# Kernel optimization log

Hardware: AMD Instinct MI355X
Metric: run time of the kernel (lower is better)

The kernel has to match this reference:

```python
import jax, jax.numpy as jnp
import numpy as np

DIM, DK, DV = 1024, 128, 128

def setup_inputs() -> dict:
    key = jax.random.key(0)
    ks = jax.random.split(key, 7)
    X = jax.random.normal(ks[0], (4, 4096, DIM), dtype=jnp.float32)
    s = DIM ** -0.5
    Wq = jax.random.normal(ks[1], (DIM, DK), dtype=jnp.float32) * s
    bq = jnp.zeros((DK,), dtype=jnp.float32)
    Wk = jax.random.normal(ks[2], (DIM, DK), dtype=jnp.float32) * s
    bk = jnp.zeros((DK,), dtype=jnp.float32)
    Wv = jax.random.normal(ks[3], (DIM, DV), dtype=jnp.float32) * s
    bv = jnp.zeros((DV,), dtype=jnp.float32)
    return {"X": X, "Wq": Wq, "bq": bq, "Wk": Wk, "bk": bk, "Wv": Wv, "bv": bv}

def reference(X, Wq, bq, Wk, bk, Wv, bv):
    scale = DK ** -0.5
    q = X @ Wq + bq              # [B, S, dk]
    k = X @ Wk + bk              # [B, S, dk]
    v = X @ Wv + bv              # [B, S, dv]
    attn = jnp.einsum('bqd,bkd->bqk', q, k) * scale  # [B, S, S]
    attn = jax.nn.softmax(attn, axis=-1)
    return jnp.einsum('bqk,bkd->bqd', attn, v)       # [B, S, dv]
```

## Files before the change

kernel.cpp:

```cpp
#include <hip/hip_runtime.h>

#define NB 4
#define SEQ 4096
#define DIMK 1024
#define DKV 128
#define SCALE 0.08838834764831845f

typedef float  f32x4  __attribute__((ext_vector_type(4)));
typedef float  f32x16 __attribute__((ext_vector_type(16)));
typedef _Float16 f16x8 __attribute__((ext_vector_type(8)));

static __device__ __forceinline__ int pkrtz(float a, float b) {
    auto h = __builtin_amdgcn_cvt_pkrtz(a, b);
    return __builtin_bit_cast(int, h);
}

__global__ void prep_wt(const float* __restrict__ Wq, const float* __restrict__ Wk,
                        const float* __restrict__ Wv, _Float16* __restrict__ WT) {
    int tid = blockIdx.x * 256 + threadIdx.x;
    int n  = tid & 127;
    int k  = (tid >> 7) & 1023;
    int w3 = tid >> 17;
    const float* W = (w3 == 0) ? Wq : (w3 == 1) ? Wk : Wv;
    WT[((size_t)w3 * 128 + n) * 1024 + k] = (_Float16)W[(size_t)k * 128 + n];
}

__global__ __launch_bounds__(256) void qkv_proj(
    const float* __restrict__ X,
    const float* __restrict__ bq, const float* __restrict__ bk, const float* __restrict__ bv,
    const _Float16* __restrict__ WT,
    _Float16* __restrict__ Qh, _Float16* __restrict__ Kh, _Float16* __restrict__ VTh) {

    __shared__ __attribute__((aligned(16))) _Float16 WTs[128 * 40];
    const int t = threadIdx.x;
    const int w = t >> 6, l = t & 63;
    const int lrow = l & 15, lg = l >> 4;
    const int w3   = blockIdx.x % 3;
    const int tile = blockIdx.x / 3;
    const int r0 = tile * 64;

    f32x4 acc[8] = {};
    const float* xrow = X + (size_t)(r0 + w * 16 + lrow) * DIMK;
    const _Float16* Wbase = WT + (size_t)w3 * 128 * 1024;

    float4 xc0 = *(const float4*)(xrow + lg * 8);
    float4 xc1 = *(const float4*)(xrow + lg * 8 + 4);

    for (int k0 = 0; k0 < DIMK; k0 += 32) {
        __syncthreads();
        #pragma unroll
        for (int i = 0; i < 2; ++i) {
            int c = t + 256 * i;
            int row = c >> 2, part = c & 3;
            *(int4*)((char*)WTs + row * 80 + part * 16) =
                *(const int4*)(Wbase + (size_t)row * 1024 + k0 + part * 8);
        }
        float4 xn0, xn1;
        if (k0 + 32 < DIMK) {
            xn0 = *(const float4*)(xrow + k0 + 32 + lg * 8);
            xn1 = *(const float4*)(xrow + k0 + 32 + lg * 8 + 4);
        }
        __syncthreads();
        f16x8 a;
        a[0] = (_Float16)xc0.x; a[1] = (_Float16)xc0.y; a[2] = (_Float16)xc0.z; a[3] = (_Float16)xc0.w;
        a[4] = (_Float16)xc1.x; a[5] = (_Float16)xc1.y; a[6] = (_Float16)xc1.z; a[7] = (_Float16)xc1.w;

        #pragma unroll
        for (int n = 0; n < 8; ++n) {
            f16x8 bf = *(const f16x8*)((const char*)WTs + (n * 16 + lrow) * 80 + lg * 16);
            acc[n] = __builtin_amdgcn_mfma_f32_16x16x32_f16(a, bf, acc[n], 0, 0, 0);
        }
        xc0 = xn0; xc1 = xn1;
    }
    const float* bias = (w3 == 0) ? bq : (w3 == 1) ? bk : bv;
    #pragma unroll
    for (int n = 0; n < 8; ++n) {
        int col = n * 16 + lrow;
        float bv_ = bias[col];
        #pragma unroll
        for (int j = 0; j < 4; ++j) {
            int grow = r0 + w * 16 + lg * 4 + j;
            float val = acc[n][j] + bv_;
            if (w3 == 0) {
                Qh[(size_t)grow * DKV + col] = (_Float16)(val * SCALE);
            } else if (w3 == 1) {
                Kh[(size_t)grow * DKV + col] = (_Float16)val;
            } else {
                int b = grow >> 12, sp = grow & 4095;
                VTh[((size_t)b * DKV + col) * SEQ + sp] = (_Float16)val;
            }
        }
    }
}

__global__ __launch_bounds__(256, 2) void attn_kernel(
    const _Float16* __restrict__ Qh, const _Float16* __restrict__ Kh,
    const _Float16* __restrict__ VTh, float* __restrict__ out) {

    __shared__ __attribute__((aligned(16))) char lds[65536];

    const int t = threadIdx.x;
    const int w = t >> 6, l = t & 63;
    const int lq = l & 31;
    const int hi = l >> 5;
    const int g  = w >> 1;
    const int wg = w & 1;
    const int lt = t & 127;

    const int work = (blockIdx.x & 7) * 32 + (blockIdx.x >> 3);
    const int b  = work >> 6;
    const int qt = work & 63;
    const int q0 = qt * 64 + wg * 32;

    char* KsG = lds + g * 16384;
    char* VsG = lds + 32768 + g * 16384;

    f16x8 qf[8];
    #pragma unroll
    for (int c = 0; c < 8; ++c)
        qf[c] = *(const f16x8*)(Qh + (size_t)(b * SEQ + q0 + lq) * DKV + c * 16 + hi * 8);

    f32x16 o[4] = {};
    float m = -INFINITY, lsum = 0.f;

    for (int kt = 0; kt < 32; ++kt) {
        const int k0 = g * 2048 + kt * 64;
        __syncthreads();
        #pragma unroll
        for (int i = 0; i < 8; ++i) {
            int c = lt + 128 * i; int row = c >> 4, part = c & 15;
            *(int4*)(KsG + row * 256 + ((part * 16) ^ ((row & 7) << 4))) =
                *(const int4*)(Kh + (size_t)(b * SEQ + k0 + row) * DKV + part * 8);
        }
        #pragma unroll
        for (int i = 0; i < 8; ++i) {
            int c = lt + 128 * i; int dv = c >> 3, part = c & 7;
            *(int4*)(VsG + dv * 128 + ((part * 16) ^ ((dv & 7) << 4))) =
                *(const int4*)(VTh + (size_t)(b * DKV + dv) * SEQ + k0 + part * 8);
        }
        __syncthreads();

        f32x16 s0 = {}, s1 = {};
        #pragma unroll
        for (int c = 0; c < 8; ++c) {
            int col = c * 32 + hi * 16;
            f16x8 kf0 = *(const f16x8*)(KsG + lq * 256 + (col ^ ((lq & 7) << 4)));
            f16x8 kf1 = *(const f16x8*)(KsG + (32 + lq) * 256 + (col ^ ((lq & 7) << 4)));
            s0 = __builtin_amdgcn_mfma_f32_32x32x16_f16(kf0, qf[c], s0, 0, 0, 0);
            s1 = __builtin_amdgcn_mfma_f32_32x32x16_f16(kf1, qf[c], s1, 0, 0, 0);
        }

        float tm = -INFINITY;
        #pragma unroll
        for (int r = 0; r < 16; ++r) tm = fmaxf(tm, fmaxf(s0[r], s1[r]));
        tm = fmaxf(tm, __shfl_xor(tm, 32));

        if (__any(tm > m + 8.f)) {
            float mnew = fmaxf(m, tm);
            float corr = __expf(m - mnew);
            m = mnew;
            lsum *= corr;
            #pragma unroll
            for (int dvt = 0; dvt < 4; ++dvt) o[dvt] *= corr;
        }
        float ts = 0.f;
        #pragma unroll
        for (int r = 0; r < 16; ++r) { s0[r] = __expf(s0[r] - m); ts += s0[r]; }
        #pragma unroll
        for (int r = 0; r < 16; ++r) { s1[r] = __expf(s1[r] - m); ts += s1[r]; }
        ts += __shfl_xor(ts, 32);
        lsum += ts;

        int wv[16];
        #pragma unroll
        for (int i = 0; i < 8; ++i) wv[i]     = pkrtz(s0[2 * i], s0[2 * i + 1]);
        #pragma unroll
        for (int i = 0; i < 8; ++i) wv[8 + i] = pkrtz(s1[2 * i], s1[2 * i + 1]);

        #pragma unroll
        for (int s = 0; s < 4; ++s) {
            const int base = (s >> 1) * 8 + (s & 1) * 4;
            int x0 = __shfl_xor(wv[base + 0], 32);
            int x1 = __shfl_xor(wv[base + 1], 32);
            int x2 = __shfl_xor(wv[base + 2], 32);
            int x3 = __shfl_xor(wv[base + 3], 32);
            union { int i[4]; f16x8 v; } bu;
            bu.i[0] = hi ? x2 : wv[base + 0];
            bu.i[1] = hi ? x3 : wv[base + 1];
            bu.i[2] = hi ? wv[base + 2] : x0;
            bu.i[3] = hi ? wv[base + 3] : x1;
            #pragma unroll
            for (int dvt = 0; dvt < 4; ++dvt) {
                int row = dvt * 32 + lq;
                f16x8 vf = *(const f16x8*)(VsG + row * 128 +
                                           ((s * 32 + hi * 16) ^ ((row & 7) << 4)));
                o[dvt] = __builtin_amdgcn_mfma_f32_32x32x16_f16(vf, bu.v, o[dvt], 0, 0, 0);
            }
        }
    }

    float* obuf  = (float*)lds;
    float* mlbuf = (float*)(lds + 40960);

    __syncthreads();
    if (g == 1) {
        #pragma unroll
        for (int dvt = 0; dvt < 4; ++dvt)
            #pragma unroll
            for (int r = 0; r < 16; ++r)
                obuf[wg * 4096 + (dvt * 16 + r) * 64 + l] = o[dvt][r];
        if (l < 32) {
            mlbuf[(wg * 32 + l) * 2 + 0] = m;
            mlbuf[(wg * 32 + l) * 2 + 1] = lsum;
        }
    }
    __syncthreads();
    if (g == 0) {
        float mo  = mlbuf[(wg * 32 + lq) * 2 + 0];
        float lo_ = mlbuf[(wg * 32 + lq) * 2 + 1];
        float mn = fmaxf(m, mo);
        float ca = __expf(m - mn);
        float cb = __expf(mo - mn);
        float rl = 1.0f / (lsum * ca + lo_ * cb);
        #pragma unroll
        for (int dvt = 0; dvt < 4; ++dvt)
            #pragma unroll
            for (int r = 0; r < 16; ++r)
                o[dvt][r] = (o[dvt][r] * ca + obuf[wg * 4096 + (dvt * 16 + r) * 64 + l] * cb) * rl;
    }
    __syncthreads();
    float* tbuf = (float*)lds;
    if (g == 0) {
        #pragma unroll
        for (int dvt = 0; dvt < 4; ++dvt)
            #pragma unroll
            for (int r = 0; r < 16; ++r) {
                int dv = dvt * 32 + (r & 3) + 8 * (r >> 2) + 4 * hi;
                tbuf[(wg * 32 + lq) * 132 + dv] = o[dvt][r];
            }
    }
    __syncthreads();
    const size_t obase = (size_t)(b * SEQ + qt * 64) * DKV;
    int row = t >> 2, c0 = (t & 3) * 32;
    #pragma unroll
    for (int i = 0; i < 8; ++i) {
        float4 v = *(const float4*)(tbuf + row * 132 + c0 + i * 4);
        *(float4*)(out + obase + row * 128 + c0 + i * 4) = v;
    }
}

extern "C" void kernel_launch(void* const* d_in, const int* in_sizes, int n_in,
                              void* d_out, int out_size, void* d_ws, size_t ws_size,
                              hipStream_t stream) {
    const float* X  = (const float*)d_in[0];
    const float* Wq = (const float*)d_in[1];
    const float* bq = (const float*)d_in[2];
    const float* Wk = (const float*)d_in[3];
    const float* bk = (const float*)d_in[4];
    const float* Wv = (const float*)d_in[5];
    const float* bv = (const float*)d_in[6];
    float* out = (float*)d_out;

    const size_t nqe = (size_t)NB * SEQ * DKV;
    _Float16* Qh  = (_Float16*)d_ws;
    _Float16* Kh  = Qh  + nqe;
    _Float16* VTh = Kh  + nqe;
    _Float16* WTh = VTh + nqe;

    prep_wt<<<(3 * 1024 * 128) / 256, 256, 0, stream>>>(Wq, Wk, Wv, WTh);
    qkv_proj<<<(NB * SEQ / 64) * 3, 256, 0, stream>>>(X, bq, bk, bv, WTh, Qh, Kh, VTh);
    attn_kernel<<<NB * 64, 256, 0, stream>>>(Qh, Kh, VTh, out);
}
```

Before: 134.7 us.

## Split KV across four waves per 32-query block with private LDS tiles

Each block now handles 32 queries instead of 64, and all four waves work on the same queries, each covering a quarter of the key sequence in its own private LDS K/V region. This removes the per-iteration __syncthreads barriers and doubles the grid to 512 blocks for better CU occupancy. The cost is a two-stage cross-wave reduction of the online-softmax partials at the end, plus each K/V tile being reused by fewer queries, which raises L2 and global traffic.

```diff
diff --git a/kernel.cpp b/kernel.cpp
--- a/kernel.cpp
+++ b/kernel.cpp
@@ -103,17 +103,14 @@
     const int w = t >> 6, l = t & 63;
     const int lq = l & 31;
     const int hi = l >> 5;
-    const int g  = w >> 1;
-    const int wg = w & 1;
-    const int lt = t & 127;
-
-    const int work = (blockIdx.x & 7) * 32 + (blockIdx.x >> 3);
-    const int b  = work >> 6;
-    const int qt = work & 63;
-    const int q0 = qt * 64 + wg * 32;
-
-    char* KsG = lds + g * 16384;
-    char* VsG = lds + 32768 + g * 16384;
+
+    const int work = (blockIdx.x & 7) * 64 + (blockIdx.x >> 3);
+    const int b  = work >> 7;
+    const int qt = work & 127;
+    const int q0 = qt * 32;
+
+    char* Kw = lds + w * 16384;
+    char* Vw = Kw + 8192;
 
     f16x8 qf[8];
     #pragma unroll
@@ -124,35 +121,34 @@
     float m = -INFINITY, lsum = 0.f;
 
     for (int kt = 0; kt < 32; ++kt) {
-        const int k0 = g * 2048 + kt * 64;
-        __syncthreads();
+        const int k0 = w * 1024 + kt * 32;
+
         #pragma unroll
         for (int i = 0; i < 8; ++i) {
-            int c = lt + 128 * i; int row = c >> 4, part = c & 15;
-            *(int4*)(KsG + row * 256 + ((part * 16) ^ ((row & 7) << 4))) =
+            int c = l + 64 * i; int row = c >> 4, part = c & 15;
+            *(int4*)(Kw + row * 256 + ((part * 16) ^ ((row & 7) << 4))) =
                 *(const int4*)(Kh + (size_t)(b * SEQ + k0 + row) * DKV + part * 8);
         }
         #pragma unroll
         for (int i = 0; i < 8; ++i) {
-            int c = lt + 128 * i; int dv = c >> 3, part = c & 7;
-            *(int4*)(VsG + dv * 128 + ((part * 16) ^ ((dv & 7) << 4))) =
-                *(const int4*)(VTh + (size_t)(b * DKV + dv) * SEQ + k0 + part * 8);
-        }
-        __syncthreads();
-
-        f32x16 s0 = {}, s1 = {};
+            int c = l + 64 * i; int dv = c >> 2, p = c & 3;
+            *(int4*)(Vw + dv * 64 + ((p ^ ((dv >> 1) & 3)) * 16)) =
+                *(const int4*)(VTh + (size_t)(b * DKV + dv) * SEQ + k0 + p * 8);
+        }
+        asm volatile("s_waitcnt lgkmcnt(0)" ::: "memory");
+        __builtin_amdgcn_sched_barrier(0);
+
+        f32x16 s = {};
         #pragma unroll
         for (int c = 0; c < 8; ++c) {
-            int col = c * 32 + hi * 16;
-            f16x8 kf0 = *(const f16x8*)(KsG + lq * 256 + (col ^ ((lq & 7) << 4)));
-            f16x8 kf1 = *(const f16x8*)(KsG + (32 + lq) * 256 + (col ^ ((lq & 7) << 4)));
-            s0 = __builtin_amdgcn_mfma_f32_32x32x16_f16(kf0, qf[c], s0, 0, 0, 0);
-            s1 = __builtin_amdgcn_mfma_f32_32x32x16_f16(kf1, qf[c], s1, 0, 0, 0);
+            f16x8 kf = *(const f16x8*)(Kw + lq * 256 +
+                                       (((2 * c + hi) * 16) ^ ((lq & 7) << 4)));
+            s = __builtin_amdgcn_mfma_f32_32x32x16_f16(kf, qf[c], s, 0, 0, 0);
         }
 
         float tm = -INFINITY;
         #pragma unroll
-        for (int r = 0; r < 16; ++r) tm = fmaxf(tm, fmaxf(s0[r], s1[r]));
+        for (int r = 0; r < 16; ++r) tm = fmaxf(tm, s[r]);
         tm = fmaxf(tm, __shfl_xor(tm, 32));
 
         if (__any(tm > m + 8.f)) {
@@ -165,21 +161,17 @@
         }
         float ts = 0.f;
         #pragma unroll
-        for (int r = 0; r < 16; ++r) { s0[r] = __expf(s0[r] - m); ts += s0[r]; }
-        #pragma unroll
-        for (int r = 0; r < 16; ++r) { s1[r] = __expf(s1[r] - m); ts += s1[r]; }
+        for (int r = 0; r < 16; ++r) { s[r] = __expf(s[r] - m); ts += s[r]; }
         ts += __shfl_xor(ts, 32);
         lsum += ts;
 
-        int wv[16];
-        #pragma unroll
-        for (int i = 0; i < 8; ++i) wv[i]     = pkrtz(s0[2 * i], s0[2 * i + 1]);
-        #pragma unroll
-        for (int i = 0; i < 8; ++i) wv[8 + i] = pkrtz(s1[2 * i], s1[2 * i + 1]);
-
-        #pragma unroll
-        for (int s = 0; s < 4; ++s) {
-            const int base = (s >> 1) * 8 + (s & 1) * 4;
+        int wv[8];
+        #pragma unroll
+        for (int i = 0; i < 8; ++i) wv[i] = pkrtz(s[2 * i], s[2 * i + 1]);
+
+        #pragma unroll
+        for (int s_ = 0; s_ < 2; ++s_) {
+            const int base = s_ * 4;
             int x0 = __shfl_xor(wv[base + 0], 32);
             int x1 = __shfl_xor(wv[base + 1], 32);
             int x2 = __shfl_xor(wv[base + 2], 32);
@@ -192,32 +184,61 @@
             #pragma unroll
             for (int dvt = 0; dvt < 4; ++dvt) {
                 int row = dvt * 32 + lq;
-                f16x8 vf = *(const f16x8*)(VsG + row * 128 +
-                                           ((s * 32 + hi * 16) ^ ((row & 7) << 4)));
+                f16x8 vf = *(const f16x8*)(Vw + row * 64 +
+                                           (((s_ * 2 + hi) ^ ((row >> 1) & 3)) * 16));
                 o[dvt] = __builtin_amdgcn_mfma_f32_32x32x16_f16(vf, bu.v, o[dvt], 0, 0, 0);
             }
         }
     }
 
     float* obuf  = (float*)lds;
-    float* mlbuf = (float*)(lds + 40960);
-
-    __syncthreads();
-    if (g == 1) {
-        #pragma unroll
-        for (int dvt = 0; dvt < 4; ++dvt)
-            #pragma unroll
-            for (int r = 0; r < 16; ++r)
-                obuf[wg * 4096 + (dvt * 16 + r) * 64 + l] = o[dvt][r];
+    float* mlbuf = (float*)(lds + 49152);
+
+    __syncthreads();
+    if (w == 1 || w == 3) {
+        int sb = (w == 3);
+        #pragma unroll
+        for (int dvt = 0; dvt < 4; ++dvt)
+            #pragma unroll
+            for (int r = 0; r < 16; ++r)
+                obuf[sb * 4096 + (dvt * 16 + r) * 64 + l] = o[dvt][r];
         if (l < 32) {
-            mlbuf[(wg * 32 + l) * 2 + 0] = m;
-            mlbuf[(wg * 32 + l) * 2 + 1] = lsum;
-        }
-    }
-    __syncthreads();
-    if (g == 0) {
-        float mo  = mlbuf[(wg * 32 + lq) * 2 + 0];
-        float lo_ = mlbuf[(wg * 32 + lq) * 2 + 1];
+            mlbuf[sb * 64 + l * 2 + 0] = m;
+            mlbuf[sb * 64 + l * 2 + 1] = lsum;
+        }
+    }
+    __syncthreads();
+    if (w == 0 || w == 2) {
+        int sb = (w == 2);
+        float mo  = mlbuf[sb * 64 + lq * 2 + 0];
+        float lo_ = mlbuf[sb * 64 + lq * 2 + 1];
+        float mn = fmaxf(m, mo);
+        float ca = __expf(m - mn);
+        float cb = __expf(mo - mn);
+        m = mn;
+        lsum = lsum * ca + lo_ * cb;
+        #pragma unroll
+        for (int dvt = 0; dvt < 4; ++dvt)
+            #pragma unroll
+            for (int r = 0; r < 16; ++r)
+                o[dvt][r] = o[dvt][r] * ca + obuf[sb * 4096 + (dvt * 16 + r) * 64 + l] * cb;
+    }
+    __syncthreads();
+    if (w == 2) {
+        #pragma unroll
+        for (int dvt = 0; dvt < 4; ++dvt)
+            #pragma unroll
+            for (int r = 0; r < 16; ++r)
+                obuf[(dvt * 16 + r) * 64 + l] = o[dvt][r];
+        if (l < 32) {
+            mlbuf[l * 2 + 0] = m;
+            mlbuf[l * 2 + 1] = lsum;
+        }
+    }
+    __syncthreads();
+    if (w == 0) {
+        float mo  = mlbuf[lq * 2 + 0];
+        float lo_ = mlbuf[lq * 2 + 1];
         float mn = fmaxf(m, mo);
         float ca = __expf(m - mn);
         float cb = __expf(mo - mn);
@@ -226,24 +247,24 @@
         for (int dvt = 0; dvt < 4; ++dvt)
             #pragma unroll
             for (int r = 0; r < 16; ++r)
-                o[dvt][r] = (o[dvt][r] * ca + obuf[wg * 4096 + (dvt * 16 + r) * 64 + l] * cb) * rl;
+                o[dvt][r] = (o[dvt][r] * ca + obuf[(dvt * 16 + r) * 64 + l] * cb) * rl;
     }
     __syncthreads();
     float* tbuf = (float*)lds;
-    if (g == 0) {
+    if (w == 0) {
         #pragma unroll
         for (int dvt = 0; dvt < 4; ++dvt)
             #pragma unroll
             for (int r = 0; r < 16; ++r) {
                 int dv = dvt * 32 + (r & 3) + 8 * (r >> 2) + 4 * hi;
-                tbuf[(wg * 32 + lq) * 132 + dv] = o[dvt][r];
+                tbuf[lq * 132 + dv] = o[dvt][r];
             }
     }
     __syncthreads();
-    const size_t obase = (size_t)(b * SEQ + qt * 64) * DKV;
-    int row = t >> 2, c0 = (t & 3) * 32;
+    const size_t obase = (size_t)(b * SEQ + qt * 32) * DKV;
+    int row = t >> 3, c0 = (t & 7) * 16;
     #pragma unroll
-    for (int i = 0; i < 8; ++i) {
+    for (int i = 0; i < 4; ++i) {
         float4 v = *(const float4*)(tbuf + row * 132 + c0 + i * 4);
         *(float4*)(out + obase + row * 128 + c0 + i * 4) = v;
     }
@@ -269,5 +290,5 @@
 
     prep_wt<<<(3 * 1024 * 128) / 256, 256, 0, stream>>>(Wq, Wk, Wv, WTh);
     qkv_proj<<<(NB * SEQ / 64) * 3, 256, 0, stream>>>(X, bq, bk, bv, WTh, Qh, Kh, VTh);
-    attn_kernel<<<NB * 64, 256, 0, stream>>>(Qh, Kh, VTh, out);
-}
+    attn_kernel<<<NB * 128, 256, 0, stream>>>(Qh, Kh, VTh, out);
+}
```

Result: faster. 124.8 us (-7.3%).
